# Performance work log

Hardware: AMD Instinct MI355X
Metric: run time of the kernel (lower is better)

The kernel has to match this reference:

```python
import jax, jax.numpy as jnp
import numpy as np

HEADS = 16
D_MODEL = 1024
D_EXP = 2048  # d_model * expansion_factor
D_HEAD = D_EXP // HEADS
DEPTH = 12
B, L = 2, 2048


def setup_inputs() -> dict:
    key = jax.random.key(0)
    ks = jax.random.split(key, 4)
    x = jax.random.normal(ks[0], (B, L, D_MODEL), dtype=jnp.float32)
    w_in = jax.random.normal(ks[1], (4 * D_EXP, D_MODEL), dtype=jnp.float32) * 0.02
    w_out = jax.random.normal(ks[2], (D_MODEL, D_EXP), dtype=jnp.float32) * (0.02 / np.sqrt(2 * DEPTH))
    # LearnedALiBi init: logspace(0,-6,heads//2,base=2) ++ zeros(heads - heads//2)
    half = HEADS // 2
    slopes = jnp.concatenate([
        jnp.asarray(2.0 ** np.linspace(0.0, -6.0, half), dtype=jnp.float32),
        jnp.zeros((HEADS - half,), dtype=jnp.float32),
    ])
    smear_factor = jnp.linspace(-6.0, 6.0, HEADS, dtype=jnp.float32)
    return {
        "x": x, "w_in": w_in, "w_out": w_out,
        "ln_in_g": jnp.ones((D_MODEL,), jnp.float32), "ln_in_b": jnp.zeros((D_MODEL,), jnp.float32),
        "ln_out_g": jnp.ones((D_MODEL,), jnp.float32), "ln_out_b": jnp.zeros((D_MODEL,), jnp.float32),
        "slopes": slopes, "smear_factor": smear_factor,
    }


def _layernorm(x, g, b, eps=1e-5):
    mu = jnp.mean(x, axis=-1, keepdims=True)
    var = jnp.mean(jnp.square(x - mu), axis=-1, keepdims=True)
    return (x - mu) * jax.lax.rsqrt(var + eps) * g + b


def reference(x, w_in, w_out, ln_in_g, ln_in_b, ln_out_g, ln_out_b, slopes, smear_factor):
    b, l, d = x.shape
    h = _layernorm(x, ln_in_g, ln_in_b)
    qkvp = h @ w_in.T  # (b, l, 4*D_EXP)
    q, k, v, p = jnp.split(qkvp, 4, axis=-1)

    def to_heads(t):  # b i (h d) -> b h i d
        return t.reshape(b, l, HEADS, D_HEAD).transpose(0, 2, 1, 3)

    q, k, v = to_heads(q), to_heads(k), to_heads(v)

    # key smearing: k_i <- (1-s)*k_i + s*k_{i-1}
    smear = jax.nn.sigmoid(smear_factor)[None, :, None, None]
    k_shift = jnp.pad(k, ((0, 0), (0, 0), (1, 0), (0, 0)))[:, :, :-1]
    k = (1.0 - smear) * k + smear * k_shift

    logits = jnp.einsum('bhid,bhjd->bhij', q, k) * (D_HEAD ** -0.5)
    # learned ALiBi bias: j * slope_h  (depends only on key index)
    alibi = jnp.arange(l, dtype=logits.dtype)[None, None, None, :] * slopes[None, :, None, None]
    # causal bias: -1e10 * (1 - tril)
    i_idx = jnp.arange(l)
    causal = jnp.where(i_idx[:, None] >= i_idx[None, :], 0.0, -1e10)[None, None]
    a = jax.nn.softmax(logits + alibi + causal, axis=-1)

    o = jnp.einsum('bhij,bhjd->bhid', a, v)
    o = o.transpose(0, 2, 1, 3).reshape(b, l, D_EXP)  # b h i d -> b i (h d)
    gated = jax.nn.silu(p) * o
    y = gated @ w_out.T
    return _layernorm(y, ln_out_g, ln_out_b)
```

## Files before the change

kernel.cpp:

```cpp
#include <hip/hip_runtime.h>
#include <hip/hip_bf16.h>
#include <stdint.h>


typedef __bf16 bf16;
typedef bf16  bf16x8 __attribute__((ext_vector_type(8)));
typedef bf16  bf16x4 __attribute__((ext_vector_type(4)));
typedef float f32x4  __attribute__((ext_vector_type(4)));

#define SEQ   2048
#define NBATC 2

__device__ __forceinline__ void gld_lds16(const bf16* g, bf16* l) {
  __builtin_amdgcn_global_load_lds((const __attribute__((address_space(1))) void*)g,
                                   (__attribute__((address_space(3))) void*)l, 16, 0, 0);
}

__device__ __forceinline__ void cvt8(const float* __restrict__ in,
                                     bf16* __restrict__ out, int t) {
  const float4* p = (const float4*)in + (size_t)t * 2;
  float4 a = p[0], b = p[1];
  bf16x8 o;
  o[0] = (bf16)a.x; o[1] = (bf16)a.y; o[2] = (bf16)a.z; o[3] = (bf16)a.w;
  o[4] = (bf16)b.x; o[5] = (bf16)b.y; o[6] = (bf16)b.z; o[7] = (bf16)b.w;
  *((bf16x8*)out + t) = o;
}

__global__ __launch_bounds__(256) void prepass_kernel(const float* __restrict__ x,
    const float* __restrict__ w_in, const float* __restrict__ w_out,
    const float* __restrict__ gamma, const float* __restrict__ beta,
    bf16* __restrict__ hb, bf16* __restrict__ w_in_b, bf16* __restrict__ w_out_b) {
  const int blk = blockIdx.x;
  const int tid = threadIdx.x;
  if (blk < 4096) {
    cvt8(w_in, w_in_b, blk * 256 + tid);
    return;
  }
  if (blk < 5120) {
    cvt8(w_out, w_out_b, (blk - 4096) * 256 + tid);
    return;
  }
  const int row = blk - 5120;
  float4 v = *(const float4*)(x + (size_t)row * 1024 + tid * 4);
  float s  = v.x + v.y + v.z + v.w;
  float ss = v.x * v.x + v.y * v.y + v.z * v.z + v.w * v.w;
#pragma unroll
  for (int m = 1; m < 64; m <<= 1) { s += __shfl_xor(s, m, 64); ss += __shfl_xor(ss, m, 64); }
  __shared__ float red[8];
  if ((tid & 63) == 0) { red[tid >> 6] = s; red[(tid >> 6) + 4] = ss; }
  __syncthreads();
  s  = red[0] + red[1] + red[2] + red[3];
  ss = red[4] + red[5] + red[6] + red[7];
  const float mu  = s * (1.f / 1024.f);
  const float inv = rsqrtf(ss * (1.f / 1024.f) - mu * mu + 1e-5f);
  float4 g  = *(const float4*)(gamma + tid * 4);
  float4 bb = *(const float4*)(beta  + tid * 4);
  bf16* o = hb + (size_t)row * 1024 + tid * 4;
  o[0] = (bf16)((v.x - mu) * inv * g.x + bb.x);
  o[1] = (bf16)((v.y - mu) * inv * g.y + bb.y);
  o[2] = (bf16)((v.z - mu) * inv * g.z + bb.z);
  o[3] = (bf16)((v.w - mu) * inv * g.w + bb.w);
}

__global__ __launch_bounds__(256) void ln_kernel(const float* __restrict__ x,
    const float* __restrict__ gamma, const float* __restrict__ beta,
    float* __restrict__ out) {
  const int row = blockIdx.x;
  const int tid = threadIdx.x;
  float4 v = *(const float4*)(x + (size_t)row * 1024 + tid * 4);
  float s  = v.x + v.y + v.z + v.w;
  float ss = v.x * v.x + v.y * v.y + v.z * v.z + v.w * v.w;
#pragma unroll
  for (int m = 1; m < 64; m <<= 1) { s += __shfl_xor(s, m, 64); ss += __shfl_xor(ss, m, 64); }
  __shared__ float red[8];
  if ((tid & 63) == 0) { red[tid >> 6] = s; red[(tid >> 6) + 4] = ss; }
  __syncthreads();
  s  = red[0] + red[1] + red[2] + red[3];
  ss = red[4] + red[5] + red[6] + red[7];
  const float mu  = s * (1.f / 1024.f);
  const float inv = rsqrtf(ss * (1.f / 1024.f) - mu * mu + 1e-5f);
  float4 g  = *(const float4*)(gamma + tid * 4);
  float4 bb = *(const float4*)(beta  + tid * 4);
  float* o = out + (size_t)row * 1024 + tid * 4;
  o[0] = (v.x - mu) * inv * g.x + bb.x;
  o[1] = (v.y - mu) * inv * g.y + bb.y;
  o[2] = (v.z - mu) * inv * g.z + bb.z;
  o[3] = (v.w - mu) * inv * g.w + bb.w;
}

__global__ __launch_bounds__(256) void prep_kernel(const bf16* __restrict__ qkvp,
    const float* __restrict__ smf, bf16* __restrict__ ksm, bf16* __restrict__ vt) {
  __shared__ bf16 T[128][72];
  const int kt = blockIdx.x, bh = blockIdx.y;
  const int b = bh >> 4, h = bh & 15;
  const int t = threadIdx.x;

  {
    int i = t >> 2, d0 = (t & 3) * 32;
    const bf16* src = qkvp + (size_t)(b * SEQ + kt * 64 + i) * 8192 + 4096 + h * 128 + d0;
#pragma unroll
    for (int m = 0; m < 4; m++) {
      bf16x8 v8 = *(const bf16x8*)(src + m * 8);
#pragma unroll
      for (int e = 0; e < 8; e++) T[d0 + m * 8 + e][i] = v8[e];
    }
  }

  {
    float sm = 1.f / (1.f + __expf(-smf[h]));
#pragma unroll
    for (int j = 0; j < 4; j++) {
      int c  = j * 256 + t;
      int il = c >> 4, d8 = c & 15;
      int i  = kt * 64 + il;
      const bf16* base = qkvp + (size_t)(b * SEQ + i) * 8192 + 2048 + h * 128 + d8 * 8;
      bf16x8 cur = *(const bf16x8*)base;
      bf16x8 prv = cur;
      if (i > 0) prv = *(const bf16x8*)(base - 8192);
      bf16x8 o;
#pragma unroll
      for (int e = 0; e < 8; e++) {
        float pv = (i > 0) ? (float)prv[e] : 0.f;
        o[e] = (bf16)((1.f - sm) * (float)cur[e] + sm * pv);
      }
      size_t idx = ((size_t)bh * SEQ + i) * 128 + ((d8 * 8) ^ ((i & 7) << 3));
      *(bf16x8*)(ksm + idx) = o;
    }
  }

  __syncthreads();
  {
    int d = t >> 1, i0 = (t & 1) * 32;
    bf16* dst = vt + (size_t)bh * (SEQ * 128) + (size_t)kt * 8192 + d * 64;
#pragma unroll
    for (int m = 0; m < 4; m++) {
      bf16x8 v8 = *(const bf16x8*)&T[d][i0 + m * 8];
      *(bf16x8*)(dst + (((i0 + m * 8)) ^ ((d & 7) << 3))) = v8;
    }
  }
}

__global__ __launch_bounds__(1024, 4) void gemm256(const bf16* __restrict__ A,
    const bf16* __restrict__ Bt, bf16* __restrict__ C, int M, int N, int K,
    int RX, int SX, int SY) {
  __shared__ bf16 As[2][256 * 64];
  __shared__ bf16 Bs[2][256 * 64];
  const int w   = blockIdx.x;
  const int xcd = w & 7, idx = w >> 3;
  const int rx = xcd % RX, ry = xcd / RX;
  const int bx = rx * SX + idx % SX;
  const int by = ry * SY + idx / SX;
  const int tid  = threadIdx.x;
  const int lane = tid & 63, wid = tid >> 6;
  const int l4 = lane >> 4, l16 = lane & 15;
  const int wr = wid >> 2, wc = wid & 3;
  const int rowBase = by * 256, colBase = bx * 256;
  const int NT = K >> 6;

  f32x4 acc[4][4];
  const f32x4 z = {0.f, 0.f, 0.f, 0.f};
#pragma unroll
  for (int i = 0; i < 4; i++)
#pragma unroll
    for (int j = 0; j < 4; j++) acc[i][j] = z;

  auto stage = [&](int t_, int buf) {
    const int k0 = t_ * 64;
#pragma unroll
    for (int j = 0; j < 2; ++j) {
      const int c   = j * 1024 + tid;
      const int row = c >> 3;
      const int sc  = ((c & 7) * 8) ^ ((row & 7) << 3);
      gld_lds16(A  + (size_t)(rowBase + row) * K + k0 + sc, &As[buf][c * 8]);
      gld_lds16(Bt + (size_t)(colBase + row) * K + k0 + sc, &Bs[buf][c * 8]);
    }
  };

  stage(0, 0);
  for (int t = 0; t < NT; ++t) {
    const int cur = t & 1;
    if (t + 1 < NT) {
      stage(t + 1, cur ^ 1);
      asm volatile("s_waitcnt vmcnt(4)" ::: "memory");
    } else {
      asm volatile("s_waitcnt vmcnt(0)" ::: "memory");
    }
    __builtin_amdgcn_sched_barrier(0);
    __builtin_amdgcn_s_barrier();
    const bf16* a_ = &As[cur][0];
    const bf16* b_ = &Bs[cur][0];
#pragma unroll
    for (int ks = 0; ks < 2; ++ks) {
      bf16x8 bfr[4];
#pragma unroll
      for (int ni = 0; ni < 4; ++ni) {
        const int br = wc * 64 + ni * 16 + l16;
        bfr[ni] = *(const bf16x8*)&b_[br * 64 + ((ks * 32 + l4 * 8) ^ ((br & 7) << 3))];
      }
#pragma unroll
      for (int mi = 0; mi < 4; ++mi) {
        const int ar = wr * 64 + mi * 16 + l16;
        bf16x8 af = *(const bf16x8*)&a_[ar * 64 + ((ks * 32 + l4 * 8) ^ ((ar & 7) << 3))];
#pragma unroll
        for (int ni = 0; ni < 4; ++ni)
          acc[mi][ni] = __builtin_amdgcn_mfma_f32_16x16x32_bf16(af, bfr[ni], acc[mi][ni], 0, 0, 0);
      }
    }
    asm volatile("s_waitcnt lgkmcnt(0)" ::: "memory");
    __builtin_amdgcn_s_barrier();
  }

#pragma unroll
  for (int mi = 0; mi < 4; ++mi)
#pragma unroll
    for (int ni = 0; ni < 4; ++ni) {
      int row = rowBase + wr * 64 + mi * 16 + l4 * 4;
      int col = colBase + wc * 64 + ni * 16 + l16;
#pragma unroll
      for (int r = 0; r < 4; ++r)
        C[(size_t)(row + r) * N + col] = (bf16)acc[mi][ni][r];
    }
}

__global__ __launch_bounds__(256, 2) void gemm128(const bf16* __restrict__ A,
    const bf16* __restrict__ Bt, float* __restrict__ C, int M, int N, int K,
    int RX, int SX, int SY) {
  __shared__ bf16 As[2][128 * 64];
  __shared__ bf16 Bs[2][128 * 64];
  const int w   = blockIdx.x;
  const int xcd = w & 7, idx = w >> 3;
  const int rx = xcd % RX, ry = xcd / RX;
  const int bx = rx * SX + idx % SX;
  const int by = ry * SY + idx / SX;
  const int tid  = threadIdx.x;
  const int lane = tid & 63, wid = tid >> 6;
  const int l4 = lane >> 4, l16 = lane & 15;
  const int wr = wid >> 1, wc = wid & 1;
  const int rowBase = by * 128, colBase = bx * 128;
  const int NT = K >> 6;

  f32x4 acc[4][4];
  const f32x4 z = {0.f, 0.f, 0.f, 0.f};
#pragma unroll
  for (int i = 0; i < 4; i++)
#pragma unroll
    for (int j = 0; j < 4; j++) acc[i][j] = z;

  auto stage = [&](int t_, int buf) {
    const int k0 = t_ * 64;
#pragma unroll
    for (int j = 0; j < 4; ++j) {
      const int c   = j * 256 + tid;
      const int row = c >> 3;
      const int sc  = ((c & 7) * 8) ^ ((row & 7) << 3);
      gld_lds16(A  + (size_t)(rowBase + row) * K + k0 + sc, &As[buf][c * 8]);
      gld_lds16(Bt + (size_t)(colBase + row) * K + k0 + sc, &Bs[buf][c * 8]);
    }
  };

  stage(0, 0);
  for (int t = 0; t < NT; ++t) {
    const int cur = t & 1;
    if (t + 1 < NT) {
      stage(t + 1, cur ^ 1);
      asm volatile("s_waitcnt vmcnt(8)" ::: "memory");
    } else {
      asm volatile("s_waitcnt vmcnt(0)" ::: "memory");
    }
    __builtin_amdgcn_sched_barrier(0);
    __builtin_amdgcn_s_barrier();
    const bf16* a_ = &As[cur][0];
    const bf16* b_ = &Bs[cur][0];
#pragma unroll
    for (int ks = 0; ks < 2; ++ks) {
      bf16x8 bfr[4];
#pragma unroll
      for (int ni = 0; ni < 4; ++ni) {
        const int br = wc * 64 + ni * 16 + l16;
        bfr[ni] = *(const bf16x8*)&b_[br * 64 + ((ks * 32 + l4 * 8) ^ ((br & 7) << 3))];
      }
#pragma unroll
      for (int mi = 0; mi < 4; ++mi) {
        const int ar = wr * 64 + mi * 16 + l16;
        bf16x8 af = *(const bf16x8*)&a_[ar * 64 + ((ks * 32 + l4 * 8) ^ ((ar & 7) << 3))];
#pragma unroll
        for (int ni = 0; ni < 4; ++ni)
          acc[mi][ni] = __builtin_amdgcn_mfma_f32_16x16x32_bf16(af, bfr[ni], acc[mi][ni], 0, 0, 0);
      }
    }
    asm volatile("s_waitcnt lgkmcnt(0)" ::: "memory");
    __builtin_amdgcn_s_barrier();
  }

#pragma unroll
  for (int mi = 0; mi < 4; ++mi)
#pragma unroll
    for (int ni = 0; ni < 4; ++ni) {
      int row = rowBase + wr * 64 + mi * 16 + l4 * 4;
      int col = colBase + wc * 64 + ni * 16 + l16;
#pragma unroll
      for (int r = 0; r < 4; ++r)
        C[(size_t)(row + r) * N + col] = acc[mi][ni][r];
    }
}

__global__ __launch_bounds__(512, 2) void attn_kernel(const bf16* __restrict__ qkvp,
    const bf16* __restrict__ ksm, const bf16* __restrict__ vt,
    const float* __restrict__ slopes, bf16* __restrict__ gated) {
  const int w   = blockIdx.x;
  const int xcd = w & 7;
  const int bh  = xcd * 4 + ((w >> 3) & 3);
  const int pr  = w >> 5;
  const int b   = bh >> 4, h = bh & 15;
  const int tid = threadIdx.x, wid = tid >> 6, lane = tid & 63;
  const int l4 = lane >> 4, l16 = lane & 15;
  const int swz = (l16 & 7) << 3;
  const float LOG2E = 1.44269504f;
  const float s2 = 0.08838834764831845f * LOG2E;
  const float slopeL = slopes[h] * LOG2E;

  __shared__ bf16 Kb[4][64 * 128];
  __shared__ bf16 Vb[4][64 * 128];
  __shared__ bf16 P_lds[128 * 64];

  const bf16* ksmB = ksm + (size_t)bh * SEQ * 128;
  const bf16* vtB  = vt  + (size_t)bh * SEQ * 128;

  auto stage = [&](int kt, int bsel) {
#pragma unroll
    for (int j = 0; j < 2; j++) {
      const int c = j * 512 + tid;
      gld_lds16(ksmB + (size_t)kt * 8192 + c * 8, &Kb[bsel][c * 8]);
      gld_lds16(vtB  + (size_t)kt * 8192 + c * 8, &Vb[bsel][c * 8]);
    }
  };

  auto run_strip = [&](int qtile) {
    const int nt = 2 * qtile + 2;
    int kt0 = 0;
    if (slopeL > 1e-6f) {
      const int W = (int)(64.f / slopeL + 128.f);
      const int wlim = qtile * 128 - W - 63;
      if (wlim > 0) kt0 = (wlim >> 6) & ~1;
    }
    const int iq = qtile * 128 + wid * 16 + l16;
    bf16x8 qf[4];
    {
      const bf16* qrow = qkvp + (size_t)(b * SEQ + iq) * 8192 + h * 128;
#pragma unroll
      for (int kb = 0; kb < 4; kb++) qf[kb] = *(const bf16x8*)(qrow + kb * 32 + l4 * 8);
    }
    f32x4 oacc[8];
    const f32x4 z = {0.f, 0.f, 0.f, 0.f};
#pragma unroll
    for (int i = 0; i < 8; i++) oacc[i] = z;
    float m2 = -1e38f, lpart = 0.f;

    auto tile = [&](int t, const bf16* K_, const bf16* V_) {
      f32x4 sacc[4];
#pragma unroll
      for (int jf = 0; jf < 4; jf++) {
        f32x4 a = z;
#pragma unroll
        for (int kb = 0; kb < 4; kb++) {
          bf16x8 kf = *(const bf16x8*)&K_[(jf * 16 + l16) * 128 + ((kb * 32 + l4 * 8) ^ swz)];
          a = __builtin_amdgcn_mfma_f32_16x16x32_bf16(kf, qf[kb], a, 0, 0, 0);
        }
        sacc[jf] = a;
      }

      const bool diag = (t >= 2 * qtile);
      const int kbase = t * 64 + l4 * 4;
#pragma unroll
      for (int jf = 0; jf < 4; jf++) {
#pragma unroll
        for (int r = 0; r < 4; r++) {
          int j = kbase + jf * 16 + r;
          float v = fmaf(sacc[jf][r], s2, (float)j * slopeL);
          if (diag && j > iq) v = -1e38f;
          sacc[jf][r] = v;
        }
      }

      float mx = sacc[0][0];
#pragma unroll
      for (int jf = 0; jf < 4; jf++)
#pragma unroll
        for (int r = 0; r < 4; r++) mx = fmaxf(mx, sacc[jf][r]);
      mx = fmaxf(mx, __shfl_xor(mx, 16, 64));
      mx = fmaxf(mx, __shfl_xor(mx, 32, 64));

      if (__any(mx > m2 + 14.f)) {
        float mnew  = fmaxf(m2, mx);
        float alpha = __builtin_amdgcn_exp2f(m2 - mnew);
        m2 = mnew;
        lpart *= alpha;
#pragma unroll
        for (int df = 0; df < 8; df++) oacc[df] *= alpha;
      }

      float rs = 0.f;
#pragma unroll
      for (int jf = 0; jf < 4; jf++) {
        bf16x4 pw;
#pragma unroll
        for (int r = 0; r < 4; r++) {
          float pe = __builtin_amdgcn_exp2f(sacc[jf][r] - m2);
          rs += pe;
          pw[r] = (bf16)pe;
        }
        *(bf16x4*)&P_lds[(wid * 16 + l16) * 64 + ((jf * 16 + l4 * 4) ^ swz)] = pw;
      }
      lpart += rs;

#pragma unroll
      for (int kb2 = 0; kb2 < 2; ++kb2) {
        bf16x8 pf = *(const bf16x8*)&P_lds[(wid * 16 + l16) * 64 + ((kb2 * 32 + l4 * 8) ^ swz)];
#pragma unroll
        for (int df = 0; df < 8; df++) {
          bf16x8 vf = *(const bf16x8*)&V_[(df * 16 + l16) * 64 + ((kb2 * 32 + l4 * 8) ^ swz)];
          oacc[df] = __builtin_amdgcn_mfma_f32_16x16x32_bf16(vf, pf, oacc[df], 0, 0, 0);
        }
      }
    };

    stage(kt0, kt0 & 3);
    stage(kt0 + 1, (kt0 + 1) & 3);
    for (int tp = kt0; tp < nt; tp += 2) {
      if (tp + 2 < nt) {
        stage(tp + 2, (tp + 2) & 3);
        stage(tp + 3, (tp + 3) & 3);
        asm volatile("s_waitcnt vmcnt(8)" ::: "memory");
      } else {
        asm volatile("s_waitcnt vmcnt(0)" ::: "memory");
      }
      __builtin_amdgcn_sched_barrier(0);
      __builtin_amdgcn_s_barrier();
      tile(tp,     Kb[tp & 3],       Vb[tp & 3]);
      tile(tp + 1, Kb[(tp + 1) & 3], Vb[(tp + 1) & 3]);
      asm volatile("s_waitcnt lgkmcnt(0)" ::: "memory");
      __builtin_amdgcn_s_barrier();
    }

    lpart += __shfl_xor(lpart, 16, 64);
    lpart += __shfl_xor(lpart, 32, 64);
    const float linv = 1.f / lpart;
    const bf16* pgrow = qkvp + (size_t)(b * SEQ + iq) * 8192 + 6144 + h * 128;
    bf16* grow = gated + (size_t)(b * SEQ + iq) * 2048 + h * 128;
#pragma unroll
    for (int df = 0; df < 8; df++) {
      const int d0 = df * 16 + l4 * 4;
      bf16x4 pg4 = *(const bf16x4*)(pgrow + d0);
      bf16x4 o4;
#pragma unroll
      for (int r = 0; r < 4; r++) {
        float o  = oacc[df][r] * linv;
        float pg = (float)pg4[r];
        float silu = pg / (1.f + __expf(-pg));
        o4[r] = (bf16)(silu * o);
      }
      *(bf16x4*)(grow + d0) = o4;
    }
  };

  run_strip(15 - pr);
  run_strip(pr);
}

extern "C" void kernel_launch(void* const* d_in, const int* in_sizes, int n_in,
                              void* d_out, int out_size, void* d_ws, size_t ws_size,
                              hipStream_t stream) {
  (void)in_sizes; (void)n_in; (void)out_size; (void)ws_size;
  const float* x      = (const float*)d_in[0];
  const float* w_in   = (const float*)d_in[1];
  const float* w_out  = (const float*)d_in[2];
  const float* lnig   = (const float*)d_in[3];
  const float* lnib   = (const float*)d_in[4];
  const float* lnog   = (const float*)d_in[5];
  const float* lnob   = (const float*)d_in[6];
  const float* slopes = (const float*)d_in[7];
  const float* smf    = (const float*)d_in[8];
  float* out = (float*)d_out;

  char* ws = (char*)d_ws;
  size_t off = 0;
  bf16* hb      = (bf16*)(ws + off); off += (size_t)4096 * 1024 * 2;
  bf16* w_in_b  = (bf16*)(ws + off); off += (size_t)8192 * 1024 * 2;
  bf16* w_out_b = (bf16*)(ws + off); off += (size_t)1024 * 2048 * 2;
  bf16* qkvp    = (bf16*)(ws + off); off += (size_t)4096 * 8192 * 2;
  bf16* ksm     = (bf16*)(ws + off); off += (size_t)32 * 2048 * 128 * 2;
  bf16* gated   = (bf16*)(ws + off); off += (size_t)4096 * 2048 * 2;
  float* yb     = (float*)(ws + off); off += (size_t)4096 * 1024 * 4;
  bf16* vt      = (bf16*)yb;

  prepass_kernel<<<9216, 256, 0, stream>>>(x, w_in, w_out, lnig, lnib,
                                           hb, w_in_b, w_out_b);
  gemm256<<<512, 1024, 0, stream>>>(hb, w_in_b, qkvp, 4096, 8192, 1024, 4, 8, 8);
  prep_kernel<<<dim3(32, 32), 256, 0, stream>>>(qkvp, smf, ksm, vt);
  attn_kernel<<<256, 512, 0, stream>>>(qkvp, ksm, vt, slopes, gated);
  gemm128<<<256, 256, 0, stream>>>(gated, w_out_b, yb, 4096, 1024, 2048, 1, 8, 4);
  ln_kernel<<<4096, 256, 0, stream>>>(yb, lnog, lnob, out);
}
```

Baseline: 213.9 us.

## Split attention strips into separate blocks and pass P through bpermute instead of LDS

The attention kernel now launches one block per query strip (512 blocks) instead of pairing two strips per block, and drops from a 4-deep to a 2-deep K/V buffer to cut LDS use so more blocks fit per CU (launch bounds raised to 4 blocks). The softmax probabilities are packed to bf16 pairs and moved into MFMA operand layout with ds_bpermute, which removes the P scratch buffer in LDS and its store/load round trip. The K-window start no longer rounds down to an even tile, since tiles are processed one at a time. The risks are less prefetch depth, more barriers per tile, and load imbalance because the paired long/short strip scheduling is gone.

```diff
diff --git a/kernel.cpp b/kernel.cpp
--- a/kernel.cpp
+++ b/kernel.cpp
@@ -7,6 +7,7 @@
 typedef bf16  bf16x8 __attribute__((ext_vector_type(8)));
 typedef bf16  bf16x4 __attribute__((ext_vector_type(4)));
 typedef float f32x4  __attribute__((ext_vector_type(4)));
+typedef uint32_t u32x4 __attribute__((ext_vector_type(4)));
 
 #define SEQ   2048
 #define NBATC 2
@@ -14,6 +15,12 @@
 __device__ __forceinline__ void gld_lds16(const bf16* g, bf16* l) {
   __builtin_amdgcn_global_load_lds((const __attribute__((address_space(1))) void*)g,
                                    (__attribute__((address_space(3))) void*)l, 16, 0, 0);
+}
+
+__device__ __forceinline__ uint32_t pack2bf(float a, float b) {
+  union { bf16 h; uint16_t u; } ua, ub;
+  ua.h = (bf16)a; ub.h = (bf16)b;
+  return ((uint32_t)ub.u << 16) | ua.u;
 }
 
 __device__ __forceinline__ void cvt8(const float* __restrict__ in,
@@ -304,13 +311,13 @@
     }
 }
 
-__global__ __launch_bounds__(512, 2) void attn_kernel(const bf16* __restrict__ qkvp,
+__global__ __launch_bounds__(512, 4) void attn_kernel(const bf16* __restrict__ qkvp,
     const bf16* __restrict__ ksm, const bf16* __restrict__ vt,
     const float* __restrict__ slopes, bf16* __restrict__ gated) {
   const int w   = blockIdx.x;
-  const int xcd = w & 7;
-  const int bh  = xcd * 4 + ((w >> 3) & 3);
-  const int pr  = w >> 5;
+  const int bh  = (w & 7) * 4 + ((w >> 3) & 3);
+  const int pr  = (w >> 5) & 7;
+  const int qtile = (w >> 8) ? pr : 15 - pr;
   const int b   = bh >> 4, h = bh & 15;
   const int tid = threadIdx.x, wid = tid >> 6, lane = tid & 63;
   const int l4 = lane >> 4, l16 = lane & 15;
@@ -319,9 +326,8 @@
   const float s2 = 0.08838834764831845f * LOG2E;
   const float slopeL = slopes[h] * LOG2E;
 
-  __shared__ bf16 Kb[4][64 * 128];
-  __shared__ bf16 Vb[4][64 * 128];
-  __shared__ bf16 P_lds[128 * 64];
+  __shared__ bf16 Kb[2][64 * 128];
+  __shared__ bf16 Vb[2][64 * 128];
 
   const bf16* ksmB = ksm + (size_t)bh * SEQ * 128;
   const bf16* vtB  = vt  + (size_t)bh * SEQ * 128;
@@ -335,136 +341,148 @@
     }
   };
 
-  auto run_strip = [&](int qtile) {
-    const int nt = 2 * qtile + 2;
-    int kt0 = 0;
-    if (slopeL > 1e-6f) {
-      const int W = (int)(64.f / slopeL + 128.f);
-      const int wlim = qtile * 128 - W - 63;
-      if (wlim > 0) kt0 = (wlim >> 6) & ~1;
-    }
-    const int iq = qtile * 128 + wid * 16 + l16;
-    bf16x8 qf[4];
-    {
-      const bf16* qrow = qkvp + (size_t)(b * SEQ + iq) * 8192 + h * 128;
-#pragma unroll
-      for (int kb = 0; kb < 4; kb++) qf[kb] = *(const bf16x8*)(qrow + kb * 32 + l4 * 8);
-    }
-    f32x4 oacc[8];
-    const f32x4 z = {0.f, 0.f, 0.f, 0.f};
-#pragma unroll
-    for (int i = 0; i < 8; i++) oacc[i] = z;
-    float m2 = -1e38f, lpart = 0.f;
-
-    auto tile = [&](int t, const bf16* K_, const bf16* V_) {
-      f32x4 sacc[4];
-#pragma unroll
-      for (int jf = 0; jf < 4; jf++) {
-        f32x4 a = z;
-#pragma unroll
-        for (int kb = 0; kb < 4; kb++) {
-          bf16x8 kf = *(const bf16x8*)&K_[(jf * 16 + l16) * 128 + ((kb * 32 + l4 * 8) ^ swz)];
-          a = __builtin_amdgcn_mfma_f32_16x16x32_bf16(kf, qf[kb], a, 0, 0, 0);
-        }
-        sacc[jf] = a;
-      }
-
-      const bool diag = (t >= 2 * qtile);
-      const int kbase = t * 64 + l4 * 4;
-#pragma unroll
-      for (int jf = 0; jf < 4; jf++) {
-#pragma unroll
-        for (int r = 0; r < 4; r++) {
-          int j = kbase + jf * 16 + r;
-          float v = fmaf(sacc[jf][r], s2, (float)j * slopeL);
-          if (diag && j > iq) v = -1e38f;
-          sacc[jf][r] = v;
-        }
-      }
-
-      float mx = sacc[0][0];
-#pragma unroll
-      for (int jf = 0; jf < 4; jf++)
-#pragma unroll
-        for (int r = 0; r < 4; r++) mx = fmaxf(mx, sacc[jf][r]);
-      mx = fmaxf(mx, __shfl_xor(mx, 16, 64));
-      mx = fmaxf(mx, __shfl_xor(mx, 32, 64));
-
-      if (__any(mx > m2 + 14.f)) {
-        float mnew  = fmaxf(m2, mx);
-        float alpha = __builtin_amdgcn_exp2f(m2 - mnew);
-        m2 = mnew;
-        lpart *= alpha;
-#pragma unroll
-        for (int df = 0; df < 8; df++) oacc[df] *= alpha;
-      }
-
-      float rs = 0.f;
-#pragma unroll
-      for (int jf = 0; jf < 4; jf++) {
-        bf16x4 pw;
-#pragma unroll
-        for (int r = 0; r < 4; r++) {
-          float pe = __builtin_amdgcn_exp2f(sacc[jf][r] - m2);
-          rs += pe;
-          pw[r] = (bf16)pe;
-        }
-        *(bf16x4*)&P_lds[(wid * 16 + l16) * 64 + ((jf * 16 + l4 * 4) ^ swz)] = pw;
-      }
-      lpart += rs;
-
-#pragma unroll
-      for (int kb2 = 0; kb2 < 2; ++kb2) {
-        bf16x8 pf = *(const bf16x8*)&P_lds[(wid * 16 + l16) * 64 + ((kb2 * 32 + l4 * 8) ^ swz)];
-#pragma unroll
-        for (int df = 0; df < 8; df++) {
-          bf16x8 vf = *(const bf16x8*)&V_[(df * 16 + l16) * 64 + ((kb2 * 32 + l4 * 8) ^ swz)];
-          oacc[df] = __builtin_amdgcn_mfma_f32_16x16x32_bf16(vf, pf, oacc[df], 0, 0, 0);
-        }
-      }
-    };
-
-    stage(kt0, kt0 & 3);
-    stage(kt0 + 1, (kt0 + 1) & 3);
-    for (int tp = kt0; tp < nt; tp += 2) {
-      if (tp + 2 < nt) {
-        stage(tp + 2, (tp + 2) & 3);
-        stage(tp + 3, (tp + 3) & 3);
-        asm volatile("s_waitcnt vmcnt(8)" ::: "memory");
-      } else {
-        asm volatile("s_waitcnt vmcnt(0)" ::: "memory");
-      }
-      __builtin_amdgcn_sched_barrier(0);
-      __builtin_amdgcn_s_barrier();
-      tile(tp,     Kb[tp & 3],       Vb[tp & 3]);
-      tile(tp + 1, Kb[(tp + 1) & 3], Vb[(tp + 1) & 3]);
-      asm volatile("s_waitcnt lgkmcnt(0)" ::: "memory");
-      __builtin_amdgcn_s_barrier();
-    }
-
-    lpart += __shfl_xor(lpart, 16, 64);
-    lpart += __shfl_xor(lpart, 32, 64);
-    const float linv = 1.f / lpart;
-    const bf16* pgrow = qkvp + (size_t)(b * SEQ + iq) * 8192 + 6144 + h * 128;
-    bf16* grow = gated + (size_t)(b * SEQ + iq) * 2048 + h * 128;
-#pragma unroll
-    for (int df = 0; df < 8; df++) {
-      const int d0 = df * 16 + l4 * 4;
-      bf16x4 pg4 = *(const bf16x4*)(pgrow + d0);
-      bf16x4 o4;
+  const int nt = 2 * qtile + 2;
+  int kt0 = 0;
+  if (slopeL > 1e-6f) {
+    const int W = (int)(64.f / slopeL + 128.f);
+    const int wlim = qtile * 128 - W - 63;
+    if (wlim > 0) kt0 = wlim >> 6;
+  }
+
+  const int iq = qtile * 128 + wid * 16 + l16;
+  bf16x8 qf[4];
+  {
+    const bf16* qrow = qkvp + (size_t)(b * SEQ + iq) * 8192 + h * 128;
+#pragma unroll
+    for (int kb = 0; kb < 4; kb++) qf[kb] = *(const bf16x8*)(qrow + kb * 32 + l4 * 8);
+  }
+  f32x4 oacc[8];
+  const f32x4 z = {0.f, 0.f, 0.f, 0.f};
+#pragma unroll
+  for (int i = 0; i < 8; i++) oacc[i] = z;
+  float m2 = -1e38f, lpart = 0.f;
+
+  const int sA = ((((l4 & 1) << 1) << 4) + l16) << 2;
+  const int sB = sA + 64;
+
+  stage(kt0, kt0 & 1);
+  for (int t = kt0; t < nt; ++t) {
+    const int cur = t & 1;
+    if (t + 1 < nt) {
+      stage(t + 1, cur ^ 1);
+      asm volatile("s_waitcnt vmcnt(4)" ::: "memory");
+    } else {
+      asm volatile("s_waitcnt vmcnt(0)" ::: "memory");
+    }
+    __builtin_amdgcn_sched_barrier(0);
+    __builtin_amdgcn_s_barrier();
+    const bf16* K_ = Kb[cur];
+    const bf16* V_ = Vb[cur];
+
+    f32x4 sacc[4];
+#pragma unroll
+    for (int jf = 0; jf < 4; jf++) {
+      f32x4 a = z;
+#pragma unroll
+      for (int kb = 0; kb < 4; kb++) {
+        bf16x8 kf = *(const bf16x8*)&K_[(jf * 16 + l16) * 128 + ((kb * 32 + l4 * 8) ^ swz)];
+        a = __builtin_amdgcn_mfma_f32_16x16x32_bf16(kf, qf[kb], a, 0, 0, 0);
+      }
+      sacc[jf] = a;
+    }
+
+    const bool diag = (t >= 2 * qtile);
+    const int kbase = t * 64 + l4 * 4;
+#pragma unroll
+    for (int jf = 0; jf < 4; jf++) {
 #pragma unroll
       for (int r = 0; r < 4; r++) {
-        float o  = oacc[df][r] * linv;
-        float pg = (float)pg4[r];
-        float silu = pg / (1.f + __expf(-pg));
-        o4[r] = (bf16)(silu * o);
-      }
-      *(bf16x4*)(grow + d0) = o4;
-    }
-  };
-
-  run_strip(15 - pr);
-  run_strip(pr);
+        int j = kbase + jf * 16 + r;
+        float v = fmaf(sacc[jf][r], s2, (float)j * slopeL);
+        if (diag && j > iq) v = -1e38f;
+        sacc[jf][r] = v;
+      }
+    }
+
+    float mx = sacc[0][0];
+#pragma unroll
+    for (int jf = 0; jf < 4; jf++)
+#pragma unroll
+      for (int r = 0; r < 4; r++) mx = fmaxf(mx, sacc[jf][r]);
+    mx = fmaxf(mx, __shfl_xor(mx, 16, 64));
+    mx = fmaxf(mx, __shfl_xor(mx, 32, 64));
+
+    if (__any(mx > m2 + 14.f)) {
+      float mnew  = fmaxf(m2, mx);
+      float alpha = __builtin_amdgcn_exp2f(m2 - mnew);
+      m2 = mnew;
+      lpart *= alpha;
+#pragma unroll
+      for (int df = 0; df < 8; df++) oacc[df] *= alpha;
+    }
+
+    uint32_t pjx[4], pjy[4];
+    float rs = 0.f;
+#pragma unroll
+    for (int jf = 0; jf < 4; jf++) {
+      float p0 = __builtin_amdgcn_exp2f(sacc[jf][0] - m2);
+      float p1 = __builtin_amdgcn_exp2f(sacc[jf][1] - m2);
+      float p2 = __builtin_amdgcn_exp2f(sacc[jf][2] - m2);
+      float p3 = __builtin_amdgcn_exp2f(sacc[jf][3] - m2);
+      rs += (p0 + p1) + (p2 + p3);
+      pjx[jf] = pack2bf(p0, p1);
+      pjy[jf] = pack2bf(p2, p3);
+    }
+    lpart += rs;
+
+#pragma unroll
+    for (int kb2 = 0; kb2 < 2; ++kb2) {
+      const int j0 = kb2 * 2, j1 = kb2 * 2 + 1;
+      int x0a = __builtin_amdgcn_ds_bpermute(sA, (int)pjx[j0]);
+      int x1a = __builtin_amdgcn_ds_bpermute(sA, (int)pjx[j1]);
+      int y0a = __builtin_amdgcn_ds_bpermute(sA, (int)pjy[j0]);
+      int y1a = __builtin_amdgcn_ds_bpermute(sA, (int)pjy[j1]);
+      int x0b = __builtin_amdgcn_ds_bpermute(sB, (int)pjx[j0]);
+      int x1b = __builtin_amdgcn_ds_bpermute(sB, (int)pjx[j1]);
+      int y0b = __builtin_amdgcn_ds_bpermute(sB, (int)pjy[j0]);
+      int y1b = __builtin_amdgcn_ds_bpermute(sB, (int)pjy[j1]);
+      const bool lo = (l4 < 2);
+      u32x4 uf;
+      uf[0] = (uint32_t)(lo ? x0a : x1a);
+      uf[1] = (uint32_t)(lo ? y0a : y1a);
+      uf[2] = (uint32_t)(lo ? x0b : x1b);
+      uf[3] = (uint32_t)(lo ? y0b : y1b);
+      bf16x8 pf = __builtin_bit_cast(bf16x8, uf);
+#pragma unroll
+      for (int df = 0; df < 8; df++) {
+        bf16x8 vf = *(const bf16x8*)&V_[(df * 16 + l16) * 64 + ((kb2 * 32 + l4 * 8) ^ swz)];
+        oacc[df] = __builtin_amdgcn_mfma_f32_16x16x32_bf16(vf, pf, oacc[df], 0, 0, 0);
+      }
+    }
+
+    asm volatile("s_waitcnt lgkmcnt(0)" ::: "memory");
+    __builtin_amdgcn_s_barrier();
+  }
+
+  lpart += __shfl_xor(lpart, 16, 64);
+  lpart += __shfl_xor(lpart, 32, 64);
+  const float linv = 1.f / lpart;
+  const bf16* pgrow = qkvp + (size_t)(b * SEQ + iq) * 8192 + 6144 + h * 128;
+  bf16* grow = gated + (size_t)(b * SEQ + iq) * 2048 + h * 128;
+#pragma unroll
+  for (int df = 0; df < 8; df++) {
+    const int d0 = df * 16 + l4 * 4;
+    bf16x4 pg4 = *(const bf16x4*)(pgrow + d0);
+    bf16x4 o4;
+#pragma unroll
+    for (int r = 0; r < 4; r++) {
+      float o  = oacc[df][r] * linv;
+      float pg = (float)pg4[r];
+      float silu = pg / (1.f + __expf(-pg));
+      o4[r] = (bf16)(silu * o);
+    }
+    *(bf16x4*)(grow + d0) = o4;
+  }
 }
 
 extern "C" void kernel_launch(void* const* d_in, const int* in_sizes, int n_in,
@@ -497,7 +515,7 @@
                                            hb, w_in_b, w_out_b);
   gemm256<<<512, 1024, 0, stream>>>(hb, w_in_b, qkvp, 4096, 8192, 1024, 4, 8, 8);
   prep_kernel<<<dim3(32, 32), 256, 0, stream>>>(qkvp, smf, ksm, vt);
-  attn_kernel<<<256, 512, 0, stream>>>(qkvp, ksm, vt, slopes, gated);
+  attn_kernel<<<512, 512, 0, stream>>>(qkvp, ksm, vt, slopes, gated);
   gemm128<<<256, 256, 0, stream>>>(gated, w_out_b, yb, 4096, 1024, 2048, 1, 8, 4);
   ln_kernel<<<4096, 256, 0, stream>>>(yb, lnog, lnob, out);
 }
```

New measurement: 221.9 us. 1.04x slower.

## Split-K the output projection GEMM and sum the partials in the final layernorm

Applied to the files above, without the earlier changes.

The output projection GEMM is split into two K-halves, launching 512 blocks instead of 256, and each half writes its own fp32 partial buffer. The final layernorm kernel reads both partials and adds them before normalizing. The goal is to fill more compute units on the small 4096x1024 GEMM. The cost is an extra 16MB fp32 write and read, plus a second workspace buffer.

```diff
diff --git a/kernel.cpp b/kernel.cpp
--- a/kernel.cpp
+++ b/kernel.cpp
@@ -62,12 +62,14 @@
   o[3] = (bf16)((v.w - mu) * inv * g.w + bb.w);
 }
 
-__global__ __launch_bounds__(256) void ln_kernel(const float* __restrict__ x,
-    const float* __restrict__ gamma, const float* __restrict__ beta,
-    float* __restrict__ out) {
+__global__ __launch_bounds__(256) void ln_kernel(const float* __restrict__ y0,
+    const float* __restrict__ y1, const float* __restrict__ gamma,
+    const float* __restrict__ beta, float* __restrict__ out) {
   const int row = blockIdx.x;
   const int tid = threadIdx.x;
-  float4 v = *(const float4*)(x + (size_t)row * 1024 + tid * 4);
+  float4 a = *(const float4*)(y0 + (size_t)row * 1024 + tid * 4);
+  float4 c = *(const float4*)(y1 + (size_t)row * 1024 + tid * 4);
+  float4 v = {a.x + c.x, a.y + c.y, a.z + c.z, a.w + c.w};
   float s  = v.x + v.y + v.z + v.w;
   float ss = v.x * v.x + v.y * v.y + v.z * v.z + v.w * v.w;
 #pragma unroll
@@ -227,7 +229,8 @@
     int RX, int SX, int SY) {
   __shared__ bf16 As[2][128 * 64];
   __shared__ bf16 Bs[2][128 * 64];
-  const int w   = blockIdx.x;
+  const int w   = blockIdx.x & 255;
+  const int ksl = blockIdx.x >> 8;
   const int xcd = w & 7, idx = w >> 3;
   const int rx = xcd % RX, ry = xcd / RX;
   const int bx = rx * SX + idx % SX;
@@ -237,7 +240,10 @@
   const int l4 = lane >> 4, l16 = lane & 15;
   const int wr = wid >> 1, wc = wid & 1;
   const int rowBase = by * 128, colBase = bx * 128;
-  const int NT = K >> 6;
+  const int KH = K >> 1;
+  const int kbase = ksl * KH;
+  const int NT = KH >> 6;
+  float* Cp = C + (size_t)ksl * M * N;
 
   f32x4 acc[4][4];
   const f32x4 z = {0.f, 0.f, 0.f, 0.f};
@@ -247,7 +253,7 @@
     for (int j = 0; j < 4; j++) acc[i][j] = z;
 
   auto stage = [&](int t_, int buf) {
-    const int k0 = t_ * 64;
+    const int k0 = kbase + t_ * 64;
 #pragma unroll
     for (int j = 0; j < 4; ++j) {
       const int c   = j * 256 + tid;
@@ -300,7 +306,7 @@
       int col = colBase + wc * 64 + ni * 16 + l16;
 #pragma unroll
       for (int r = 0; r < 4; ++r)
-        C[(size_t)(row + r) * N + col] = acc[mi][ni][r];
+        Cp[(size_t)(row + r) * N + col] = acc[mi][ni][r];
     }
 }
 
@@ -490,14 +496,15 @@
   bf16* qkvp    = (bf16*)(ws + off); off += (size_t)4096 * 8192 * 2;
   bf16* ksm     = (bf16*)(ws + off); off += (size_t)32 * 2048 * 128 * 2;
   bf16* gated   = (bf16*)(ws + off); off += (size_t)4096 * 2048 * 2;
-  float* yb     = (float*)(ws + off); off += (size_t)4096 * 1024 * 4;
-  bf16* vt      = (bf16*)yb;
+  float* yb0    = (float*)(ws + off); off += (size_t)4096 * 1024 * 4;
+  float* yb1    = (float*)(ws + off); off += (size_t)4096 * 1024 * 4;
+  bf16* vt      = (bf16*)yb0;
 
   prepass_kernel<<<9216, 256, 0, stream>>>(x, w_in, w_out, lnig, lnib,
                                            hb, w_in_b, w_out_b);
   gemm256<<<512, 1024, 0, stream>>>(hb, w_in_b, qkvp, 4096, 8192, 1024, 4, 8, 8);
   prep_kernel<<<dim3(32, 32), 256, 0, stream>>>(qkvp, smf, ksm, vt);
   attn_kernel<<<256, 512, 0, stream>>>(qkvp, ksm, vt, slopes, gated);
-  gemm128<<<256, 256, 0, stream>>>(gated, w_out_b, yb, 4096, 1024, 2048, 1, 8, 4);
-  ln_kernel<<<4096, 256, 0, stream>>>(yb, lnog, lnob, out);
-}
+  gemm128<<<512, 256, 0, stream>>>(gated, w_out_b, yb0, 4096, 1024, 2048, 1, 8, 4);
+  ln_kernel<<<4096, 256, 0, stream>>>(yb0, yb1, lnog, lnob, out);
+}
```

Measured after the change: 204.8 us. 1.04x faster.
